# Performance work log

Hardware: AMD Instinct MI355X
Metric: run time of the kernel (lower is better)

Reference implementation:

```python
import jax, jax.numpy as jnp
import numpy as np

D_MODEL = 2048
H_Q = 32
H_KV = 8
D_HEAD = D_MODEL // H_Q  # 64
Q_PER_KV = H_Q // H_KV   # 4
B, L = 2, 2048


def setup_inputs() -> dict:
    key = jax.random.key(0)
    kx, kq, kk, kv, ko = jax.random.split(key, 5)
    s = 0.02
    return {
        "x": jax.random.normal(kx, (B, L, D_MODEL), dtype=jnp.float32),
        "Wq": jax.random.normal(kq, (D_MODEL, D_MODEL), dtype=jnp.float32) * s,
        "Wk": jax.random.normal(kk, (D_MODEL, D_HEAD * H_KV), dtype=jnp.float32) * s,
        "Wv": jax.random.normal(kv, (D_MODEL, D_HEAD * H_KV), dtype=jnp.float32) * s,
        "Wo": jax.random.normal(ko, (D_MODEL, D_MODEL), dtype=jnp.float32) * s,
    }


def reference(x, Wq, Wk, Wv, Wo):
    Bb, Ll, _ = x.shape
    # Projections (nn.Linear with bias=False -> x @ W; weights stored as (in, out))
    Q = (x @ Wq).reshape(Bb, Ll, H_Q, D_HEAD)          # (B, L, Hq, d)
    K = (x @ Wk).reshape(Bb, Ll, H_KV, D_HEAD)         # (B, L, Hkv, d)
    V = (x @ Wv).reshape(Bb, Ll, H_KV, D_HEAD)
    # Group query heads: (B, Hkv, q_per_kv, L, d)
    Q = Q.transpose(0, 2, 1, 3).reshape(Bb, H_KV, Q_PER_KV, Ll, D_HEAD)
    K = K.transpose(0, 2, 1, 3)                        # (B, Hkv, L, d)
    V = V.transpose(0, 2, 1, 3)
    scale = 1.0 / jnp.sqrt(jnp.asarray(D_HEAD, dtype=x.dtype))
    # scores: (B, Hkv, q_per_kv, L, L)
    scores = jnp.einsum('bhgqd,bhkd->bhgqk', Q, K) * scale
    attn = jax.nn.softmax(scores, axis=-1)
    out = jnp.einsum('bhgqk,bhkd->bhgqd', attn, V)     # (B, Hkv, g, L, d)
    out = out.reshape(Bb, H_Q, Ll, D_HEAD).transpose(0, 2, 1, 3).reshape(Bb, Ll, D_MODEL)
    return out @ Wo
```

## Files before the change

### kernel.cpp

```cpp
#include <hip/hip_runtime.h>
#include <hip/hip_bf16.h>
#include <cstdint>
#include <cmath>

#define D_MODEL 2048
#define HQ 32
#define HKV 8
#define DH 64
#define NB 2
#define LSEQ 2048
#define MROWS (NB*LSEQ)
#define KVB 64

typedef __attribute__((ext_vector_type(8))) short short8;
typedef __attribute__((ext_vector_type(4))) float f32x4;
typedef __attribute__((ext_vector_type(4))) unsigned short ushort4v;
typedef __attribute__((ext_vector_type(4))) unsigned int uint4v;
typedef unsigned short ushort;

#if __has_builtin(__builtin_amdgcn_exp2f)
#define EXP2(x) __builtin_amdgcn_exp2f(x)
#else
#define EXP2(x) exp2f(x)
#endif

__device__ __forceinline__ ushort f2bf(float f) {
    unsigned u = __float_as_uint(f);
    u += 0x7fffu + ((u >> 16) & 1u);
    return (ushort)(u >> 16);
}

__device__ __forceinline__ unsigned cvtpk_sp(float a, float b) {
    unsigned r;
    asm("s_nop 1\n\tv_cvt_pk_bf16_f32 %0, %1, %2" : "=v"(r) : "v"(a), "v"(b));
    return r;
}

__device__ __forceinline__ void gload_lds16(const ushort* gsrc, ushort* ldst) {
    __builtin_amdgcn_global_load_lds((const __attribute__((address_space(1))) void*)gsrc,
                                     (__attribute__((address_space(3))) void*)ldst, 16, 0, 0);
}

__global__ __launch_bounds__(256)
void cvt_bf16_k(const float* __restrict__ in, ushort* __restrict__ out, int n4) {
    int i = blockIdx.x * blockDim.x + threadIdx.x;
    if (i < n4) {
        float4 v = *(const float4*)(in + (size_t)i * 4);
        ushort4v o = {f2bf(v.x), f2bf(v.y), f2bf(v.z), f2bf(v.w)};
        *(ushort4v*)(out + (size_t)i * 4) = o;
    }
}

__global__ __launch_bounds__(256)
void transpose_all(const float* __restrict__ Wq, const float* __restrict__ Wk,
                   const float* __restrict__ Wv, const float* __restrict__ Wo,
                   ushort* __restrict__ dst) {
    __shared__ float t[32][33];
    const int tid = threadIdx.x;
    const int n0 = blockIdx.x * 32, k0 = blockIdx.y * 32;
    const float* W; int Nd, nl;
    if (n0 < 2048)      { W = Wq; Nd = 2048; nl = n0; }
    else if (n0 < 2560) { W = Wk; Nd = 512;  nl = n0 - 2048; }
    else if (n0 < 3072) { W = Wv; Nd = 512;  nl = n0 - 2560; }
    else                { W = Wo; Nd = 2048; nl = n0 - 3072; }
    const int r = tid >> 3, c4 = (tid & 7) << 2;
    float4 v = *(const float4*)(W + (size_t)(k0 + r) * Nd + nl + c4);
    t[r][c4 + 0] = v.x; t[r][c4 + 1] = v.y; t[r][c4 + 2] = v.z; t[r][c4 + 3] = v.w;
    __syncthreads();
    const int n = tid >> 3, kc = (tid & 7) << 2;
    ushort4v o = {f2bf(t[kc + 0][n]), f2bf(t[kc + 1][n]), f2bf(t[kc + 2][n]), f2bf(t[kc + 3][n])};
    *(ushort4v*)(dst + (size_t)(n0 + n) * 2048 + k0 + kc) = o;
}

template<int BM, int MODE>
__global__ __launch_bounds__(256, 2)
void gemm_bf16(const ushort* __restrict__ A, const ushort* __restrict__ Bt,
               void* __restrict__ Cv, int M, int N, int K, float scale)
{
    constexpr int BN = 128;
    constexpr int FM = BM / 32;
    constexpr int ISSA = BM / 64;
    __shared__ __align__(16) ushort smem[2 * (BM + BN) * 32];
    ushort* As = smem;
    ushort* Bs = smem + 2 * BM * 32;

    const int tid = threadIdx.x;
    const int w = tid >> 6;
    const int wr = w >> 1, wc = w & 1;
    const int g = (tid & 63) >> 4, r16 = tid & 15;
    const int bm = blockIdx.y * BM, bn = blockIdx.x * BN;
    const int srow = tid >> 2, sphys = tid & 3;

    f32x4 acc[FM][4];
#pragma unroll
    for (int i = 0; i < FM; ++i)
#pragma unroll
        for (int j = 0; j < 4; ++j) acc[i][j] = {0.f, 0.f, 0.f, 0.f};

    auto stage = [&](int buf, int k0) {
#pragma unroll
        for (int i = 0; i < ISSA; ++i) {
            int row = i * 64 + srow;
            int slog = sphys ^ ((row >> 1) & 3);
            gload_lds16(A + (size_t)(bm + row) * K + k0 + slog * 8,
                        As + buf * BM * 32 + (i * 64 + w * 16) * 32);
        }
#pragma unroll
        for (int i = 0; i < 2; ++i) {
            int row = i * 64 + srow;
            int slog = sphys ^ ((row >> 1) & 3);
            gload_lds16(Bt + (size_t)(bn + row) * K + k0 + slog * 8,
                        Bs + buf * 128 * 32 + (i * 64 + w * 16) * 32);
        }
    };

    const int NTk = K >> 5;
    stage(0, 0);
    __syncthreads();
    int buf = 0;
    for (int kt = 0; kt < NTk; ++kt) {
        if (kt + 1 < NTk) stage(buf ^ 1, (kt + 1) << 5);
        const ushort* Ab = As + buf * BM * 32;
        const ushort* Bb = Bs + buf * 128 * 32;
        short8 af[FM], bfv[4];
#pragma unroll
        for (int mi = 0; mi < FM; ++mi) {
            int row = wr * (BM / 2) + mi * 16 + r16;
            int p = g ^ ((row >> 1) & 3);
            af[mi] = *(const short8*)(Ab + row * 32 + p * 8);
        }
#pragma unroll
        for (int ni = 0; ni < 4; ++ni) {
            int row = wc * 64 + ni * 16 + r16;
            int p = g ^ ((row >> 1) & 3);
            bfv[ni] = *(const short8*)(Bb + row * 32 + p * 8);
        }
#pragma unroll
        for (int mi = 0; mi < FM; ++mi)
#pragma unroll
            for (int ni = 0; ni < 4; ++ni)
                acc[mi][ni] = __builtin_amdgcn_mfma_f32_16x16x32_bf16(af[mi], bfv[ni], acc[mi][ni], 0, 0, 0);
        __syncthreads();
        buf ^= 1;
    }

    float* C = (float*)Cv;
#pragma unroll
    for (int mi = 0; mi < FM; ++mi)
#pragma unroll
        for (int ni = 0; ni < 4; ++ni)
#pragma unroll
            for (int r = 0; r < 4; ++r) {
                int row = bm + wr * (BM / 2) + mi * 16 + g * 4 + r;
                int col = bn + wc * 64 + ni * 16 + r16;
                C[(size_t)row * N + col] = acc[mi][ni][r] * scale;
            }
}

__global__ __launch_bounds__(256, 2)
void gemm_qkv(const ushort* __restrict__ A, const ushort* __restrict__ Bt,
              ushort* __restrict__ Qd, ushort* __restrict__ Kd, ushort* __restrict__ Vd,
              float qscale)
{
    constexpr int K = 2048;
    __shared__ __align__(16) ushort smem[2 * 256 * 32];

    const int tid = threadIdx.x;
    const int l = tid & 63;
    const int w = tid >> 6;
    const int wr = w >> 1, wc = w & 1;
    const int g = l >> 4, r16 = l & 15;
    const int bm = blockIdx.y * 128, bn = blockIdx.x * 128;
    const int srow = tid >> 2, sphys = tid & 3;

    ushort* As = smem;
    ushort* Bs = smem + 2 * 128 * 32;

    f32x4 acc[4][4];
#pragma unroll
    for (int i = 0; i < 4; ++i)
#pragma unroll
        for (int j = 0; j < 4; ++j) acc[i][j] = {0.f, 0.f, 0.f, 0.f};

    auto stage = [&](int buf, int k0) {
#pragma unroll
        for (int i = 0; i < 2; ++i) {
            int row = i * 64 + srow;
            int slog = sphys ^ ((row >> 1) & 3);
            gload_lds16(A + (size_t)(bm + row) * K + k0 + slog * 8,
                        As + buf * 128 * 32 + (i * 64 + w * 16) * 32);
            gload_lds16(Bt + (size_t)(bn + row) * K + k0 + slog * 8,
                        Bs + buf * 128 * 32 + (i * 64 + w * 16) * 32);
        }
    };

    stage(0, 0);
    __syncthreads();
    int buf = 0;
    for (int kt = 0; kt < K / 32; ++kt) {
        if (kt + 1 < K / 32) stage(buf ^ 1, (kt + 1) << 5);
        const ushort* Ab = As + buf * 128 * 32;
        const ushort* Bb = Bs + buf * 128 * 32;
        short8 af[4], bfv[4];
#pragma unroll
        for (int mi = 0; mi < 4; ++mi) {
            int row = wr * 64 + mi * 16 + r16;
            int p = g ^ ((row >> 1) & 3);
            af[mi] = *(const short8*)(Ab + row * 32 + p * 8);
        }
#pragma unroll
        for (int ni = 0; ni < 4; ++ni) {
            int row = wc * 64 + ni * 16 + r16;
            int p = g ^ ((row >> 1) & 3);
            bfv[ni] = *(const short8*)(Bb + row * 32 + p * 8);
        }
#pragma unroll
        for (int mi = 0; mi < 4; ++mi)
#pragma unroll
            for (int ni = 0; ni < 4; ++ni)
                acc[mi][ni] = __builtin_amdgcn_mfma_f32_16x16x32_bf16(af[mi], bfv[ni], acc[mi][ni], 0, 0, 0);
        __syncthreads();
        buf ^= 1;
    }

    const int colbase = bn + wc * 64;
    const int rowbase = bm + wr * 64;
    const int b = rowbase >> 11;
    const int l0 = rowbase & (LSEQ - 1);
    ushort* Ls = smem + w * 64 * 64;
    __syncthreads();

    if (colbase < 2560) {
        const float sc = (colbase < 2048) ? qscale : 1.f;
#pragma unroll
        for (int mi = 0; mi < 4; ++mi)
#pragma unroll
            for (int ni = 0; ni < 4; ++ni)
#pragma unroll
                for (int r = 0; r < 4; ++r)
                    Ls[(mi * 16 + g * 4 + r) * 64 + ni * 16 + r16] = f2bf(acc[mi][ni][r] * sc);
        __syncthreads();
        ushort* dst;
        if (colbase < 2048)
            dst = Qd + (((size_t)(b * 32 + (colbase >> 6))) * LSEQ + l0) * 64;
        else
            dst = Kd + (((size_t)(b * 8 + ((colbase - 2048) >> 6))) * LSEQ + l0) * 64;
#pragma unroll
        for (int c = 0; c < 8; ++c) {
            int idx = c * 64 + l;
            *(short8*)(dst + idx * 8) = *(const short8*)(Ls + idx * 8);
        }
    } else {
#pragma unroll
        for (int mi = 0; mi < 4; ++mi)
#pragma unroll
            for (int ni = 0; ni < 4; ++ni) {
                ushort4v pk = {f2bf(acc[mi][ni][0]), f2bf(acc[mi][ni][1]),
                               f2bf(acc[mi][ni][2]), f2bf(acc[mi][ni][3])};
                *(ushort4v*)(&Ls[(((mi >> 1) * 64 + ni * 16 + r16) * 4 + g) * 8 + (mi & 1) * 4]) = pk;
            }
        __syncthreads();
        const int h = (colbase - 2560) >> 6;
        ushort* dst = Vd + (((size_t)(b * 8 + h)) * 64 + (l0 >> 5)) * 2048;
#pragma unroll
        for (int c = 0; c < 8; ++c) {
            int idx = c * 64 + l;
            *(short8*)(dst + (size_t)idx * 8) = *(const short8*)(Ls + idx * 8);
        }
    }
}

__global__ __launch_bounds__(256, 2)
void attn_bf16(const ushort* __restrict__ Qb, const ushort* __restrict__ Kb,
               const ushort* __restrict__ Vtb, ushort* __restrict__ Ob)
{
    __shared__ __align__(16) ushort Ks[2][KVB * 64];
    __shared__ __align__(16) ushort Vs[2][KVB * 64];

    const int tid = threadIdx.x;
    const int l = tid & 63, w = tid >> 6;
    const int g = l >> 4, r16 = l & 15;
    const int bh = blockIdx.y, b = bh >> 5, hq = bh & 31, hk = hq >> 2;
    const int q0 = blockIdx.x * 128 + w * 32;

    const ushort* Qh = Qb + (size_t)bh * LSEQ * 64;
    const ushort* Kh = Kb + (size_t)(b * HKV + hk) * LSEQ * 64;
    const ushort* Vh = Vtb + (size_t)(b * HKV + hk) * 64 * LSEQ;

    short8 qf[2][2];
#pragma unroll
    for (int qb = 0; qb < 2; ++qb)
#pragma unroll
        for (int dh = 0; dh < 2; ++dh)
            qf[qb][dh] = *(const short8*)(Qh + (size_t)(q0 + qb * 16 + r16) * 64 + dh * 32 + g * 8);

    short8 ones;
#pragma unroll
    for (int j = 0; j < 8; ++j) ones[j] = (short)0x3F80;

    f32x4 acco[4][2];
#pragma unroll
    for (int i = 0; i < 4; ++i)
#pragma unroll
        for (int j = 0; j < 2; ++j) acco[i][j] = {0.f, 0.f, 0.f, 0.f};
    f32x4 accl[2] = {{0,0,0,0},{0,0,0,0}};

    const int sr = tid >> 3, sp = tid & 7;

    auto stage = [&](ushort* kdst, ushort* vdst, int k0) {
        const int slog = sp ^ (sr & 7);
#pragma unroll
        for (int i = 0; i < 2; ++i)
            gload_lds16(Kh + (size_t)(k0 + i * 32 + sr) * 64 + slog * 8,
                        kdst + i * 2048 + w * 512);
#pragma unroll
        for (int i = 0; i < 2; ++i)
            gload_lds16(Vh + (size_t)k0 * 64 + i * 2048 + (size_t)tid * 8,
                        vdst + i * 2048 + w * 512);
    };

    auto body = [&](const ushort* Kc, const ushort* Vc, ushort* Kn, ushort* Vn, int t) {
        if (t + 1 < LSEQ / KVB) stage(Kn, Vn, (t + 1) * KVB);

        uint4v pw[2][2];
#pragma unroll
        for (int kb = 0; kb < 4; ++kb) {
            const int row = kb * 16 + r16, c = r16 & 7;
            short8 kf0 = *(const short8*)(Kc + row * 64 + ((g) ^ c) * 8);
            short8 kf1 = *(const short8*)(Kc + row * 64 + ((4 + g) ^ c) * 8);
#pragma unroll
            for (int qb = 0; qb < 2; ++qb) {
                f32x4 z = {0.f, 0.f, 0.f, 0.f};
                z = __builtin_amdgcn_mfma_f32_16x16x32_bf16(kf0, qf[qb][0], z, 0, 0, 0);
                f32x4 sq = __builtin_amdgcn_mfma_f32_16x16x32_bf16(kf1, qf[qb][1], z, 0, 0, 0);
                float p0 = EXP2(sq[0]), p1 = EXP2(sq[1]);
                float p2 = EXP2(sq[2]), p3 = EXP2(sq[3]);
                pw[kb >> 1][qb][(kb & 1) * 2 + 0] = cvtpk_sp(p0, p1);
                pw[kb >> 1][qb][(kb & 1) * 2 + 1] = cvtpk_sp(p2, p3);
            }
        }

        short8 vf[4][2];
#pragma unroll
        for (int db = 0; db < 4; ++db)
#pragma unroll
            for (int s = 0; s < 2; ++s)
                vf[db][s] = *(const short8*)(Vc + ((s * 64 + db * 16 + r16) * 4 + g) * 8);

#pragma unroll
        for (int db = 0; db < 4; ++db)
#pragma unroll
            for (int qb = 0; qb < 2; ++qb) {
                acco[db][qb] = __builtin_amdgcn_mfma_f32_16x16x32_bf16(
                    vf[db][0], *(short8*)&pw[0][qb], acco[db][qb], 0, 0, 0);
                acco[db][qb] = __builtin_amdgcn_mfma_f32_16x16x32_bf16(
                    vf[db][1], *(short8*)&pw[1][qb], acco[db][qb], 0, 0, 0);
            }
#pragma unroll
        for (int qb = 0; qb < 2; ++qb) {
            accl[qb] = __builtin_amdgcn_mfma_f32_16x16x32_bf16(
                ones, *(short8*)&pw[0][qb], accl[qb], 0, 0, 0);
            accl[qb] = __builtin_amdgcn_mfma_f32_16x16x32_bf16(
                ones, *(short8*)&pw[1][qb], accl[qb], 0, 0, 0);
        }

        __syncthreads();
    };

    stage(Ks[0], Vs[0], 0);
    __syncthreads();
    for (int kt = 0; kt < LSEQ / KVB; kt += 2) {
        body(Ks[0], Vs[0], Ks[1], Vs[1], kt);
        body(Ks[1], Vs[1], Ks[0], Vs[0], kt + 1);
    }

    float inv[2] = {1.f / accl[0][0], 1.f / accl[1][0]};
#pragma unroll
    for (int qb = 0; qb < 2; ++qb)
#pragma unroll
        for (int db = 0; db < 4; ++db) {
            int lseq = q0 + qb * 16 + r16;
            ushort4v o = {f2bf(acco[db][qb][0] * inv[qb]), f2bf(acco[db][qb][1] * inv[qb]),
                          f2bf(acco[db][qb][2] * inv[qb]), f2bf(acco[db][qb][3] * inv[qb])};
            *(ushort4v*)(Ob + ((size_t)b * LSEQ + lseq) * D_MODEL + hq * 64 + db * 16 + g * 4) = o;
        }
}

extern "C" void kernel_launch(void* const* d_in, const int* in_sizes, int n_in,
                              void* d_out, int out_size, void* d_ws, size_t ws_size,
                              hipStream_t stream)
{
    const float* x  = (const float*)d_in[0];
    const float* Wq = (const float*)d_in[1];
    const float* Wk = (const float*)d_in[2];
    const float* Wv = (const float*)d_in[3];
    const float* Wo = (const float*)d_in[4];

    ushort* xb  = (ushort*)d_ws;
    ushort* Ob  = xb;
    ushort* Wf  = xb  + (size_t)MROWS * D_MODEL;
    ushort* Wot = Wf  + (size_t)3072 * D_MODEL;
    ushort* Kbf = Wot + (size_t)D_MODEL * D_MODEL;
    ushort* Vtb = Kbf + (size_t)NB * HKV * LSEQ * DH;
    ushort* Qbf = (ushort*)d_out;

    dim3 blk(256);
    cvt_bf16_k<<<dim3((MROWS * D_MODEL / 4 + 255) / 256), blk, 0, stream>>>(x, xb, MROWS * D_MODEL / 4);
    transpose_all<<<dim3(5120 / 32, D_MODEL / 32), blk, 0, stream>>>(Wq, Wk, Wv, Wo, Wf);

    gemm_qkv<<<dim3(3072 / 128, MROWS / 128), blk, 0, stream>>>(
        xb, Wf, Qbf, Kbf, Vtb, 0.125f * 1.44269504f);

    attn_bf16<<<dim3(LSEQ / 128, NB * HQ), blk, 0, stream>>>(Qbf, Kbf, Vtb, Ob);

    gemm_bf16<128, 0><<<dim3(D_MODEL / 128, MROWS / 128), blk, 0, stream>>>(
        Ob, Wot, d_out, MROWS, D_MODEL, D_MODEL, 1.f);
}
```

Baseline: 192.4 us.

## Merge prelude conversion kernels and add XCD-aware block swizzle to GEMMs and attention

Combines the x fp32-to-bf16 conversion and the weight transpose into one prelude launch, which removes a kernel launch and lets both run concurrently. It also remaps workgroup IDs in the QKV GEMM, output GEMM and attention kernels so that neighbouring tiles land on the same XCD. The goal is better L2 reuse of shared A/B tiles and of K/V heads. The swizzle assumes the grid size is divisible by 8, and the merged prelude mixes two block types with different shared-memory needs.

After: 187.1 us. 1.03x faster.

```diff
diff --git a/kernel.cpp b/kernel.cpp
--- a/kernel.cpp
+++ b/kernel.cpp
@@ -41,35 +41,44 @@
                                      (__attribute__((address_space(3))) void*)ldst, 16, 0, 0);
 }
 
+__device__ __forceinline__ int xcd_swz(int wgid, int nwg) {
+    const int chunk = nwg >> 3;
+    return (wgid & 7) * chunk + (wgid >> 3);
+}
+
 __global__ __launch_bounds__(256)
-void cvt_bf16_k(const float* __restrict__ in, ushort* __restrict__ out, int n4) {
-    int i = blockIdx.x * blockDim.x + threadIdx.x;
-    if (i < n4) {
-        float4 v = *(const float4*)(in + (size_t)i * 4);
-        ushort4v o = {f2bf(v.x), f2bf(v.y), f2bf(v.z), f2bf(v.w)};
-        *(ushort4v*)(out + (size_t)i * 4) = o;
+void prelude(const float* __restrict__ x, ushort* __restrict__ xb,
+             const float* __restrict__ Wq, const float* __restrict__ Wk,
+             const float* __restrict__ Wv, const float* __restrict__ Wo,
+             ushort* __restrict__ dst) {
+    const int bx = blockIdx.x;
+    const int tid = threadIdx.x;
+    if (bx < 2048) {
+        const int base = bx * 256 + tid;
+#pragma unroll
+        for (int it = 0; it < 4; ++it) {
+            const int i = base + it * 524288;
+            float4 v = *(const float4*)(x + (size_t)i * 4);
+            ushort4v o = {f2bf(v.x), f2bf(v.y), f2bf(v.z), f2bf(v.w)};
+            *(ushort4v*)(xb + (size_t)i * 4) = o;
+        }
+    } else {
+        __shared__ float t[32][33];
+        const int tt = bx - 2048;
+        const int n0 = (tt % 160) * 32, k0 = (tt / 160) * 32;
+        const float* W; int Nd, nl;
+        if (n0 < 2048)      { W = Wq; Nd = 2048; nl = n0; }
+        else if (n0 < 2560) { W = Wk; Nd = 512;  nl = n0 - 2048; }
+        else if (n0 < 3072) { W = Wv; Nd = 512;  nl = n0 - 2560; }
+        else                { W = Wo; Nd = 2048; nl = n0 - 3072; }
+        const int r = tid >> 3, c4 = (tid & 7) << 2;
+        float4 v = *(const float4*)(W + (size_t)(k0 + r) * Nd + nl + c4);
+        t[r][c4 + 0] = v.x; t[r][c4 + 1] = v.y; t[r][c4 + 2] = v.z; t[r][c4 + 3] = v.w;
+        __syncthreads();
+        const int n = tid >> 3, kc = (tid & 7) << 2;
+        ushort4v o = {f2bf(t[kc + 0][n]), f2bf(t[kc + 1][n]), f2bf(t[kc + 2][n]), f2bf(t[kc + 3][n])};
+        *(ushort4v*)(dst + (size_t)(n0 + n) * 2048 + k0 + kc) = o;
     }
-}
-
-__global__ __launch_bounds__(256)
-void transpose_all(const float* __restrict__ Wq, const float* __restrict__ Wk,
-                   const float* __restrict__ Wv, const float* __restrict__ Wo,
-                   ushort* __restrict__ dst) {
-    __shared__ float t[32][33];
-    const int tid = threadIdx.x;
-    const int n0 = blockIdx.x * 32, k0 = blockIdx.y * 32;
-    const float* W; int Nd, nl;
-    if (n0 < 2048)      { W = Wq; Nd = 2048; nl = n0; }
-    else if (n0 < 2560) { W = Wk; Nd = 512;  nl = n0 - 2048; }
-    else if (n0 < 3072) { W = Wv; Nd = 512;  nl = n0 - 2560; }
-    else                { W = Wo; Nd = 2048; nl = n0 - 3072; }
-    const int r = tid >> 3, c4 = (tid & 7) << 2;
-    float4 v = *(const float4*)(W + (size_t)(k0 + r) * Nd + nl + c4);
-    t[r][c4 + 0] = v.x; t[r][c4 + 1] = v.y; t[r][c4 + 2] = v.z; t[r][c4 + 3] = v.w;
-    __syncthreads();
-    const int n = tid >> 3, kc = (tid & 7) << 2;
-    ushort4v o = {f2bf(t[kc + 0][n]), f2bf(t[kc + 1][n]), f2bf(t[kc + 2][n]), f2bf(t[kc + 3][n])};
-    *(ushort4v*)(dst + (size_t)(n0 + n) * 2048 + k0 + kc) = o;
 }
 
 template<int BM, int MODE>
@@ -88,7 +97,8 @@
     const int w = tid >> 6;
     const int wr = w >> 1, wc = w & 1;
     const int g = (tid & 63) >> 4, r16 = tid & 15;
-    const int bm = blockIdx.y * BM, bn = blockIdx.x * BN;
+    const int sw = xcd_swz(blockIdx.y * gridDim.x + blockIdx.x, gridDim.x * gridDim.y);
+    const int bm = (sw / gridDim.x) * BM, bn = (sw % gridDim.x) * BN;
     const int srow = tid >> 2, sphys = tid & 3;
 
     f32x4 acc[FM][4];
@@ -170,7 +180,8 @@
     const int w = tid >> 6;
     const int wr = w >> 1, wc = w & 1;
     const int g = l >> 4, r16 = l & 15;
-    const int bm = blockIdx.y * 128, bn = blockIdx.x * 128;
+    const int sw = xcd_swz(blockIdx.y * gridDim.x + blockIdx.x, gridDim.x * gridDim.y);
+    const int bm = (sw / gridDim.x) * 128, bn = (sw % gridDim.x) * 128;
     const int srow = tid >> 2, sphys = tid & 3;
 
     ushort* As = smem;
@@ -280,8 +291,9 @@
     const int tid = threadIdx.x;
     const int l = tid & 63, w = tid >> 6;
     const int g = l >> 4, r16 = l & 15;
-    const int bh = blockIdx.y, b = bh >> 5, hq = bh & 31, hk = hq >> 2;
-    const int q0 = blockIdx.x * 128 + w * 32;
+    const int sw = xcd_swz(blockIdx.y * gridDim.x + blockIdx.x, gridDim.x * gridDim.y);
+    const int bh = sw / gridDim.x, b = bh >> 5, hq = bh & 31, hk = hq >> 2;
+    const int q0 = (sw % gridDim.x) * 128 + w * 32;
 
     const ushort* Qh = Qb + (size_t)bh * LSEQ * 64;
     const ushort* Kh = Kb + (size_t)(b * HKV + hk) * LSEQ * 64;
@@ -405,8 +417,7 @@
     ushort* Qbf = (ushort*)d_out;
 
     dim3 blk(256);
-    cvt_bf16_k<<<dim3((MROWS * D_MODEL / 4 + 255) / 256), blk, 0, stream>>>(x, xb, MROWS * D_MODEL / 4);
-    transpose_all<<<dim3(5120 / 32, D_MODEL / 32), blk, 0, stream>>>(Wq, Wk, Wv, Wo, Wf);
+    prelude<<<dim3(2048 + 10240), blk, 0, stream>>>(x, xb, Wq, Wk, Wv, Wo, Wf);
 
     gemm_qkv<<<dim3(3072 / 128, MROWS / 128), blk, 0, stream>>>(
         xb, Wf, Qbf, Kbf, Vtb, 0.125f * 1.44269504f);
```
